# Performance work log

Hardware: AMD Instinct MI355X
Metric: run time of the kernel (lower is better)

The kernel has to match this reference:

```python
import jax, jax.numpy as jnp
import numpy as np

N_SEQ, SEQ_LEN, HIDDEN, BATCH = 2048, 128, 128, 64


def setup_inputs() -> dict:
    key = jax.random.key(0)
    ks = jax.random.split(key, 6)
    s_ih = 1.0 / np.sqrt(SEQ_LEN)
    s_hh = 1.0 / np.sqrt(HIDDEN)
    s_fc = 1.0 / np.sqrt(N_SEQ * HIDDEN)
    return {
        "x": jax.random.normal(ks[0], (BATCH, N_SEQ, SEQ_LEN), dtype=jnp.float32),
        "h0": jnp.zeros((BATCH, HIDDEN), dtype=jnp.float32),
        "c0": jnp.zeros((BATCH, HIDDEN), dtype=jnp.float32),
        # LSTM weights, PyTorch gate order (i, f, g, o) packed on last axis
        "W_ih": jax.random.uniform(ks[1], (SEQ_LEN, 4 * HIDDEN), jnp.float32, -s_ih, s_ih),
        "W_hh": jax.random.uniform(ks[2], (HIDDEN, 4 * HIDDEN), jnp.float32, -s_hh, s_hh),
        "b": jax.random.uniform(ks[3], (4 * HIDDEN,), jnp.float32, -s_ih, s_ih),
        "fc_w": jax.random.uniform(ks[4], (2, N_SEQ * HIDDEN), jnp.float32, -s_fc, s_fc),
        "fc_b": jax.random.uniform(ks[5], (2,), jnp.float32, -s_fc, s_fc),
    }


def _lstm(x_tmajor, h0, c0, W_ih, W_hh, b):
    # x_tmajor: [T, B, D]. Precompute input projection in one big matmul.
    pre = jnp.einsum("tbd,dg->tbg", x_tmajor, W_ih) + b  # [T, B, 4H]
    H = h0.shape[-1]

    def step(carry, pre_t):
        h, c = carry
        gates = pre_t + h @ W_hh  # [B, 4H]
        i = jax.nn.sigmoid(gates[:, 0 * H:1 * H])
        f = jax.nn.sigmoid(gates[:, 1 * H:2 * H])
        g = jnp.tanh(gates[:, 2 * H:3 * H])
        o = jax.nn.sigmoid(gates[:, 3 * H:4 * H])
        c_new = f * c + i * g
        h_new = o * jnp.tanh(c_new)
        return (h_new, c_new), h_new

    (_, _), hs = jax.lax.scan(step, (h0, c0), pre)
    return hs  # [T, B, H]


def reference(x, h0, c0, W_ih, W_hh, b, fc_w, fc_b):
    xt = jnp.transpose(x, (1, 0, 2))              # [T, B, D]
    hs = _lstm(xt, h0, c0, W_ih, W_hh, b)          # [T, B, H]
    hb = jnp.transpose(hs, (1, 0, 2))              # [B, T, H]
    flat = hb.reshape(hb.shape[0], -1)             # [B, T*H]
    return flat @ fc_w.T + fc_b                    # [B, 2]
```

## Files before the change

kernel.cpp:

```cpp
#include <hip/hip_runtime.h>

#define T_SEQ 2048
#define NBATCH 64
#define DIM 128
#define HID 128
#define G4 512
#define GRP 16
#define TT 16
#define LOG2E 1.44269504088896f

typedef _Float16 h2v   __attribute__((ext_vector_type(2)));
typedef _Float16 f16x8 __attribute__((ext_vector_type(8)));
typedef float    f32x4 __attribute__((ext_vector_type(4)));

__device__ __forceinline__ unsigned pack2(float lo, float hi) {
    h2v v; v.x = (_Float16)lo; v.y = (_Float16)hi;
    return __builtin_bit_cast(unsigned, v);
}
__device__ __forceinline__ float dot2(unsigned a, unsigned b, float c) {
#if __has_builtin(__builtin_amdgcn_fdot2)
    return __builtin_amdgcn_fdot2(__builtin_bit_cast(h2v, a),
                                  __builtin_bit_cast(h2v, b), c, false);
#else
    h2v av = __builtin_bit_cast(h2v, a), bv = __builtin_bit_cast(h2v, b);
    c = fmaf((float)av.x, (float)bv.x, c);
    return fmaf((float)av.y, (float)bv.y, c);
#endif
}
__device__ __forceinline__ float rcp_(float x)  { return __builtin_amdgcn_rcpf(x); }
__device__ __forceinline__ float exp2_(float x) { return __builtin_amdgcn_exp2f(x); }
template <int CTRL>
__device__ __forceinline__ float qmov(float v) {
    int r = __builtin_amdgcn_mov_dpp(__builtin_bit_cast(int, v), CTRL, 0xF, 0xF, true);
    return __builtin_bit_cast(float, r);
}
#define QP_XOR1 0xB1
#define QP_XOR2 0x4E
#define QP_B0   0x00
#define QP_B1   0x55
#define QP_B2   0xAA
#define QP_B3   0xFF

__device__ __forceinline__ void barrier_lgkm() {
    asm volatile("s_waitcnt lgkmcnt(0)\n\ts_barrier" ::: "memory");
    __builtin_amdgcn_sched_barrier(0);
}

__global__ __launch_bounds__(256) void prep(
    const float* __restrict__ x,
    const float* __restrict__ Wih,
    const float* __restrict__ Whh,
    const float* __restrict__ bias,
    _Float16* __restrict__ x16,
    _Float16* __restrict__ aXf,
    unsigned* __restrict__ whh_pk,
    float* __restrict__ bias_s)
{
    const size_t gtid   = (size_t)blockIdx.x * blockDim.x + threadIdx.x;
    const size_t stride = (size_t)gridDim.x * blockDim.x;

    const size_t n_x2 = (size_t)NBATCH * T_SEQ * DIM / 2;
    for (size_t i = gtid; i < n_x2; i += stride) {
        float2 v = reinterpret_cast<const float2*>(x)[i];
        h2v p; p.x = (_Float16)v.x; p.y = (_Float16)v.y;
        reinterpret_cast<h2v*>(x16)[i] = p;
    }
    for (size_t n = gtid; n < 65536; n += stride) {
        int i  = (int)n & 7;
        int l  = ((int)n >> 3) & 63;
        int ks = ((int)n >> 9) & 3;
        int j  = ((int)n >> 11) & 3;
        int w  = (int)n >> 13;
        int col = l & 15, hi = l >> 4;
        int chr  = 16 * (4 * w + j) + col;
        int wcol = (chr & 3) * HID + (chr >> 2);
        float sc = ((chr & 3) == 2) ? -2.0f * LOG2E : -LOG2E;
        int k = ks * 32 + hi * 8 + i;
        aXf[n] = (_Float16)(Wih[(size_t)k * G4 + wcol] * sc);
    }
    for (size_t n = gtid; n < 32768; n += stride) {
        int tid = (int)n & 511;
        int gi  = (int)n >> 9;
        int g = gi >> 4, ii = gi & 15;
        int j = tid >> 2, q = tid & 3;
        int k0 = q * 32 + 2 * ii;
        float sc = (g == 2) ? -2.0f * LOG2E : -LOG2E;
        whh_pk[n] = pack2(Whh[(size_t)k0 * G4 + g * HID + j] * sc,
                          Whh[(size_t)(k0 + 1) * G4 + g * HID + j] * sc);
    }
    for (size_t n = gtid; n < 512; n += stride) {
        int gate = (int)n & 3, u = (int)n >> 2;
        float sc = (gate == 2) ? -2.0f * LOG2E : -LOG2E;
        bias_s[n] = bias[gate * HID + u] * sc;
    }
}

__global__ __launch_bounds__(512, 2) void pre_mfma(
    const _Float16* __restrict__ x16,
    const _Float16* __restrict__ aXf,
    const float* __restrict__ bias_s,
    _Float16* __restrict__ pre,
    int t0)
{
    const int tid = threadIdx.x;
    const int w   = tid >> 6;
    const int l   = tid & 63;
    const int col = l & 15;
    const int hi  = l >> 4;
    const int bg  = blockIdx.x & 3;
    const int lt0 = (blockIdx.x >> 2) * TT;
    const int batch = bg * 16 + col;

    f16x8 aX[4][4];
    f32x4 bv[4];
    #pragma unroll
    for (int j = 0; j < 4; ++j) {
        #pragma unroll
        for (int ks = 0; ks < 4; ++ks)
            aX[j][ks] = *reinterpret_cast<const f16x8*>(
                aXf + (((size_t)(w * 4 + j) * 4 + ks) << 9) + l * 8);
        bv[j] = *reinterpret_cast<const f32x4*>(bias_s + 64 * w + 16 * j + 4 * hi);
    }

    const _Float16* xb_base = x16 + (size_t)batch * T_SEQ * DIM + hi * 8;

    for (int tt = 0; tt < TT; ++tt) {
        const int lt = lt0 + tt;
        const int t  = t0 + lt;
        f16x8 xf[4];
        #pragma unroll
        for (int ks = 0; ks < 4; ++ks)
            xf[ks] = *reinterpret_cast<const f16x8*>(
                xb_base + (size_t)t * DIM + ks * 32);
        #pragma unroll
        for (int j = 0; j < 4; ++j) {
            f32x4 acc = bv[j];
            #pragma unroll
            for (int ks = 0; ks < 4; ++ks)
                acc = __builtin_amdgcn_mfma_f32_16x16x32_f16(aX[j][ks], xf[ks], acc, 0, 0, 0);
            uint2 o;
            o.x = pack2(acc[0], acc[1]);
            o.y = pack2(acc[2], acc[3]);
            *reinterpret_cast<uint2*>(
                pre + ((size_t)lt * NBATCH + batch) * G4 + 16 * (4 * w + j) + 4 * hi) = o;
        }
    }
}

__global__ __launch_bounds__(512, 1) void lstm_scan(
    const _Float16* __restrict__ pre,
    const unsigned* __restrict__ whh_pk,
    const float* __restrict__ h0,
    const float* __restrict__ c0,
    float* __restrict__ state,
    _Float16* __restrict__ trace,
    int t0, int tc)
{
    __shared__ __align__(16) _Float16 h_sh[2][HID];

    const int tid = threadIdx.x;
    const int j = tid >> 2;
    const int q = tid & 3;
    const int b = blockIdx.x;
    const bool q1 = (q & 1) != 0;
    const bool q2 = (q & 2) != 0;

    float* st_h = state;
    float* st_c = state + NBATCH * HID;

    unsigned wpk[4][16];
    #pragma unroll
    for (int g = 0; g < 4; ++g)
        #pragma unroll
        for (int ii = 0; ii < 16; ++ii)
            wpk[g][ii] = whh_pk[(size_t)(g * 16 + ii) * 512 + tid];

    float c, hj;
    if (t0 == 0) {
        hj = h0[b * HID + j]; c = c0[b * HID + j];
    } else {
        hj = st_h[b * HID + j];
        c  = st_c[b * HID + j];
    }
    if (q == 0) h_sh[0][j] = (_Float16)hj;

    const size_t pstep = (size_t)NBATCH * G4;
    const _Float16* pb = pre + (size_t)b * G4 + tid;
    _Float16* tb = trace + ((size_t)b * T_SEQ + t0) * HID + j;

    unsigned short prA[GRP], prB[GRP];
    #pragma unroll
    for (int s = 0; s < GRP; ++s)
        prA[s] = __builtin_bit_cast(unsigned short, pb[(size_t)s * pstep]);

    __syncthreads();

#define LOADG(PR, TGN)                                                       \
    {                                                                        \
        const int tgl = (TGN);                                               \
        _Pragma("unroll")                                                    \
        for (int s = 0; s < GRP; ++s)                                        \
            PR[s] = __builtin_bit_cast(unsigned short,                       \
                        pb[(size_t)(tgl + s) * pstep]);                      \
    }

#define STEP16(PR, TG)                                                       \
    _Pragma("unroll")                                                        \
    for (int s = 0; s < GRP; ++s) {                                          \
        const int cur = s & 1;                                               \
        const uint4* hp = reinterpret_cast<const uint4*>(&h_sh[cur][q * 32]);\
        float a0 = 0.f, a1 = 0.f, a2 = 0.f, a3 = 0.f;                        \
        _Pragma("unroll")                                                    \
        for (int m = 0; m < 4; ++m) {                                        \
            uint4 hv = hp[m];                                                \
            a0 = dot2(hv.x, wpk[0][4 * m + 0], a0);                          \
            a1 = dot2(hv.x, wpk[1][4 * m + 0], a1);                          \
            a2 = dot2(hv.x, wpk[2][4 * m + 0], a2);                          \
            a3 = dot2(hv.x, wpk[3][4 * m + 0], a3);                          \
            a0 = dot2(hv.y, wpk[0][4 * m + 1], a0);                          \
            a1 = dot2(hv.y, wpk[1][4 * m + 1], a1);                          \
            a2 = dot2(hv.y, wpk[2][4 * m + 1], a2);                          \
            a3 = dot2(hv.y, wpk[3][4 * m + 1], a3);                          \
            a0 = dot2(hv.z, wpk[0][4 * m + 2], a0);                          \
            a1 = dot2(hv.z, wpk[1][4 * m + 2], a1);                          \
            a2 = dot2(hv.z, wpk[2][4 * m + 2], a2);                          \
            a3 = dot2(hv.z, wpk[3][4 * m + 2], a3);                          \
            a0 = dot2(hv.w, wpk[0][4 * m + 3], a0);                          \
            a1 = dot2(hv.w, wpk[1][4 * m + 3], a1);                          \
            a2 = dot2(hv.w, wpk[2][4 * m + 3], a2);                          \
            a3 = dot2(hv.w, wpk[3][4 * m + 3], a3);                          \
        }                                                                    \
        float t01  = q1 ? a1 : a0;                                           \
        float t01o = q1 ? a0 : a1;                                           \
        t01 += qmov<QP_XOR1>(t01o);                                          \
        float t23  = q1 ? a3 : a2;                                           \
        float t23o = q1 ? a2 : a3;                                           \
        t23 += qmov<QP_XOR1>(t23o);                                          \
        float tq  = q2 ? t23 : t01;                                          \
        float tqo = q2 ? t01 : t23;                                          \
        tq += qmov<QP_XOR2>(tqo);                                            \
        tq += (float)__builtin_bit_cast(_Float16, PR[s]);                    \
        float v = rcp_(1.0f + exp2_(tq));                                    \
        float gi = qmov<QP_B0>(v);                                           \
        float gf = qmov<QP_B1>(v);                                           \
        float vg = qmov<QP_B2>(v);                                           \
        float go = qmov<QP_B3>(v);                                           \
        c = fmaf(gf, c, fmaf(gi + gi, vg, -gi));                             \
        float vc = rcp_(1.0f + exp2_(-2.0f * LOG2E * c));                    \
        float hn = fmaf(go + go, vc, -go);                                   \
        hj = hn;                                                             \
        _Float16 h16 = (_Float16)hn;                                         \
        if (q == 0) {                                                        \
            h_sh[cur ^ 1][j] = h16;                                          \
            tb[(size_t)((TG) + s) * HID] = h16;                              \
        }                                                                    \
        barrier_lgkm();                                                      \
    }

    for (int tg = 0; tg < tc; tg += 2 * GRP) {
        LOADG(prB, tg + GRP);
        STEP16(prA, tg);
        const int tga = (tg + 2 * GRP < tc) ? tg + 2 * GRP : tg;
        LOADG(prA, tga);
        STEP16(prB, tg + GRP);
    }
#undef LOADG
#undef STEP16

    if (t0 + tc < T_SEQ) {
        if (q == 0) { st_h[b * HID + j] = hj; st_c[b * HID + j] = c; }
    }
}

__global__ __launch_bounds__(256) void fc_part(
    const _Float16* __restrict__ trace,
    const float* __restrict__ fcw,
    float* __restrict__ part)
{
    __shared__ float red[4][2];
    const int b = blockIdx.x, ck = blockIdx.y, tid = threadIdx.x;
    const int n4 = T_SEQ * HID / 4;
    const int base = ck * n4;
    const _Float16* tbase = trace + (size_t)b * (T_SEQ * HID) + base;
    const float* w0 = fcw + base;
    const float* w1 = fcw + (size_t)T_SEQ * HID + base;

    float s0 = 0.f, s1 = 0.f;
    for (int i = tid * 8; i < n4; i += 256 * 8) {
        uint4 tv = *reinterpret_cast<const uint4*>(tbase + i);
        float wa0[8], wa1[8];
        *reinterpret_cast<float4*>(&wa0[0]) = *reinterpret_cast<const float4*>(w0 + i);
        *reinterpret_cast<float4*>(&wa0[4]) = *reinterpret_cast<const float4*>(w0 + i + 4);
        *reinterpret_cast<float4*>(&wa1[0]) = *reinterpret_cast<const float4*>(w1 + i);
        *reinterpret_cast<float4*>(&wa1[4]) = *reinterpret_cast<const float4*>(w1 + i + 4);
        const unsigned* tw = reinterpret_cast<const unsigned*>(&tv);
        #pragma unroll
        for (int e = 0; e < 4; ++e) {
            h2v hh = __builtin_bit_cast(h2v, tw[e]);
            float hx = (float)hh.x, hy = (float)hh.y;
            s0 = fmaf(hx, wa0[2 * e], s0);
            s0 = fmaf(hy, wa0[2 * e + 1], s0);
            s1 = fmaf(hx, wa1[2 * e], s1);
            s1 = fmaf(hy, wa1[2 * e + 1], s1);
        }
    }
    #pragma unroll
    for (int d = 32; d >= 1; d >>= 1) {
        s0 += __shfl_xor(s0, d);
        s1 += __shfl_xor(s1, d);
    }
    const int w = tid >> 6;
    if ((tid & 63) == 0) { red[w][0] = s0; red[w][1] = s1; }
    __syncthreads();
    if (tid < 2) {
        part[(b * 4 + ck) * 2 + tid] =
            red[0][tid] + red[1][tid] + red[2][tid] + red[3][tid];
    }
}

__global__ __launch_bounds__(128) void fc_fin(
    const float* __restrict__ part,
    const float* __restrict__ fcb,
    float* __restrict__ out)
{
    const int tid = threadIdx.x;
    const int b = tid >> 1, o = tid & 1;
    float v = part[(b * 4 + 0) * 2 + o] + part[(b * 4 + 1) * 2 + o]
            + part[(b * 4 + 2) * 2 + o] + part[(b * 4 + 3) * 2 + o];
    out[b * 2 + o] = v + fcb[o];
}

extern "C" void kernel_launch(void* const* d_in, const int* in_sizes, int n_in,
                              void* d_out, int out_size, void* d_ws, size_t ws_size,
                              hipStream_t stream) {
    const float* x    = (const float*)d_in[0];
    const float* h0   = (const float*)d_in[1];
    const float* c0   = (const float*)d_in[2];
    const float* Wih  = (const float*)d_in[3];
    const float* Whh  = (const float*)d_in[4];
    const float* bias = (const float*)d_in[5];
    const float* fcw  = (const float*)d_in[6];
    const float* fcb  = (const float*)d_in[7];
    float* out = (float*)d_out;

    char* wsb = (char*)d_ws;
    const size_t X = (size_t)NBATCH * T_SEQ * DIM * 2;
    _Float16* x16    = (_Float16*)wsb;
    _Float16* trace  = (_Float16*)(wsb + X);
    float*    state  = (float*)(wsb + 2 * X);
    float*    part   = (float*)(wsb + 2 * X + 65536);
    _Float16* aXf    = (_Float16*)(wsb + 2 * X + 65536 + 2048);
    unsigned* whh_pk = (unsigned*)(wsb + 2 * X + 65536 + 2048 + 131072);
    float*    bias_s = (float*)(wsb + 2 * X + 65536 + 2048 + 2 * 131072);
    _Float16* pre    = (_Float16*)(wsb + 2 * X + 65536 + 2048 + 2 * 131072 + 2048);

    const size_t head = 2 * X + 65536 + 2048 + 2 * 131072 + 2048;
    const size_t per_t_bytes = (size_t)NBATCH * G4 * sizeof(_Float16);
    size_t avail = (ws_size > head) ? ws_size - head : 0;
    int Tc = (int)(avail / per_t_bytes);
    Tc &= ~(2 * GRP - 1);
    if (Tc < 2 * GRP) Tc = 2 * GRP;
    if (Tc > T_SEQ) Tc = T_SEQ;

    prep<<<512, 256, 0, stream>>>(x, Wih, Whh, bias, x16, aXf, whh_pk, bias_s);
    for (int t0 = 0; t0 < T_SEQ; t0 += Tc) {
        int tc = (t0 + Tc <= T_SEQ) ? Tc : (T_SEQ - t0);
        pre_mfma<<<(tc / TT) * 4, 512, 0, stream>>>(x16, aXf, bias_s, pre, t0);
        lstm_scan<<<64, 512, 0, stream>>>(pre, whh_pk, h0, c0, state, trace, t0, tc);
    }
    fc_part<<<dim3(64, 4), 256, 0, stream>>>(trace, fcw, part);
    fc_fin<<<1, 128, 0, stream>>>(part, fcb, out);
}
```

Measured before the change: 1.076 ms.

## Split LSTM recurrent matvec across 8 lanes per hidden unit with 1024-thread blocks

The recurrent scan now uses 1024 threads per batch block, with 8 lanes per hidden unit (4 gates times 2 K-halves) instead of 4, so each lane holds 32 packed weights and does 32 dot2 ops per step instead of 64. The cross-lane reduction changes from gate-transposing quad swaps to a single xor-1 add, and gates are broadcast through a half-row mirror DPP. Weight packing in prep is reordered to match. This shortens the serial per-step latency chain. In exchange it doubles the waves taking part in every per-step barrier and adds more redundant lanes.

```diff
diff --git a/kernel.cpp b/kernel.cpp
--- a/kernel.cpp
+++ b/kernel.cpp
@@ -35,11 +35,9 @@
     return __builtin_bit_cast(float, r);
 }
 #define QP_XOR1 0xB1
-#define QP_XOR2 0x4E
 #define QP_B0   0x00
-#define QP_B1   0x55
 #define QP_B2   0xAA
-#define QP_B3   0xFF
+#define DPP_HMIR 0x141
 
 __device__ __forceinline__ void barrier_lgkm() {
     asm volatile("s_waitcnt lgkmcnt(0)\n\ts_barrier" ::: "memory");
@@ -53,7 +51,7 @@
     const float* __restrict__ bias,
     _Float16* __restrict__ x16,
     _Float16* __restrict__ aXf,
-    unsigned* __restrict__ whh_pk,
+    unsigned* __restrict__ whh_pk8,
     float* __restrict__ bias_s)
 {
     const size_t gtid   = (size_t)blockIdx.x * blockDim.x + threadIdx.x;
@@ -79,14 +77,14 @@
         aXf[n] = (_Float16)(Wih[(size_t)k * G4 + wcol] * sc);
     }
     for (size_t n = gtid; n < 32768; n += stride) {
-        int tid = (int)n & 511;
-        int gi  = (int)n >> 9;
-        int g = gi >> 4, ii = gi & 15;
-        int j = tid >> 2, q = tid & 3;
-        int k0 = q * 32 + 2 * ii;
+        int tid = (int)n & 1023;
+        int wi  = (int)n >> 10;
+        int j = tid >> 3, s = tid & 7;
+        int g = s >> 1, kh = s & 1;
+        int k0 = kh * 64 + 2 * wi;
         float sc = (g == 2) ? -2.0f * LOG2E : -LOG2E;
-        whh_pk[n] = pack2(Whh[(size_t)k0 * G4 + g * HID + j] * sc,
-                          Whh[(size_t)(k0 + 1) * G4 + g * HID + j] * sc);
+        whh_pk8[n] = pack2(Whh[(size_t)k0 * G4 + g * HID + j] * sc,
+                           Whh[(size_t)(k0 + 1) * G4 + g * HID + j] * sc);
     }
     for (size_t n = gtid; n < 512; n += stride) {
         int gate = (int)n & 3, u = (int)n >> 2;
@@ -147,9 +145,9 @@
     }
 }
 
-__global__ __launch_bounds__(512, 1) void lstm_scan(
+__global__ __launch_bounds__(1024, 1) void lstm_scan(
     const _Float16* __restrict__ pre,
-    const unsigned* __restrict__ whh_pk,
+    const unsigned* __restrict__ whh_pk8,
     const float* __restrict__ h0,
     const float* __restrict__ c0,
     float* __restrict__ state,
@@ -159,21 +157,18 @@
     __shared__ __align__(16) _Float16 h_sh[2][HID];
 
     const int tid = threadIdx.x;
-    const int j = tid >> 2;
-    const int q = tid & 3;
+    const int j  = tid >> 3;
+    const int s  = tid & 7;
+    const int kh = s & 1;
     const int b = blockIdx.x;
-    const bool q1 = (q & 1) != 0;
-    const bool q2 = (q & 2) != 0;
 
     float* st_h = state;
     float* st_c = state + NBATCH * HID;
 
-    unsigned wpk[4][16];
+    unsigned wpk[32];
     #pragma unroll
-    for (int g = 0; g < 4; ++g)
-        #pragma unroll
-        for (int ii = 0; ii < 16; ++ii)
-            wpk[g][ii] = whh_pk[(size_t)(g * 16 + ii) * 512 + tid];
+    for (int i = 0; i < 32; ++i)
+        wpk[i] = whh_pk8[(size_t)i * 1024 + tid];
 
     float c, hj;
     if (t0 == 0) {
@@ -182,16 +177,16 @@
         hj = st_h[b * HID + j];
         c  = st_c[b * HID + j];
     }
-    if (q == 0) h_sh[0][j] = (_Float16)hj;
+    if (s == 0) h_sh[0][j] = (_Float16)hj;
 
     const size_t pstep = (size_t)NBATCH * G4;
-    const _Float16* pb = pre + (size_t)b * G4 + tid;
+    const _Float16* pb = pre + (size_t)b * G4 + 4 * j + (s >> 1);
     _Float16* tb = trace + ((size_t)b * T_SEQ + t0) * HID + j;
 
     unsigned short prA[GRP], prB[GRP];
     #pragma unroll
-    for (int s = 0; s < GRP; ++s)
-        prA[s] = __builtin_bit_cast(unsigned short, pb[(size_t)s * pstep]);
+    for (int ss = 0; ss < GRP; ++ss)
+        prA[ss] = __builtin_bit_cast(unsigned short, pb[(size_t)ss * pstep]);
 
     __syncthreads();
 
@@ -199,60 +194,42 @@
     {                                                                        \
         const int tgl = (TGN);                                               \
         _Pragma("unroll")                                                    \
-        for (int s = 0; s < GRP; ++s)                                        \
-            PR[s] = __builtin_bit_cast(unsigned short,                       \
-                        pb[(size_t)(tgl + s) * pstep]);                      \
+        for (int ss = 0; ss < GRP; ++ss)                                     \
+            PR[ss] = __builtin_bit_cast(unsigned short,                      \
+                        pb[(size_t)(tgl + ss) * pstep]);                     \
     }
 
 #define STEP16(PR, TG)                                                       \
     _Pragma("unroll")                                                        \
-    for (int s = 0; s < GRP; ++s) {                                          \
-        const int cur = s & 1;                                               \
-        const uint4* hp = reinterpret_cast<const uint4*>(&h_sh[cur][q * 32]);\
+    for (int ss = 0; ss < GRP; ++ss) {                                       \
+        const int cur = ss & 1;                                              \
+        const uint4* hp = reinterpret_cast<const uint4*>(&h_sh[cur][kh * 64]);\
         float a0 = 0.f, a1 = 0.f, a2 = 0.f, a3 = 0.f;                        \
         _Pragma("unroll")                                                    \
-        for (int m = 0; m < 4; ++m) {                                        \
-            uint4 hv = hp[m];                                                \
-            a0 = dot2(hv.x, wpk[0][4 * m + 0], a0);                          \
-            a1 = dot2(hv.x, wpk[1][4 * m + 0], a1);                          \
-            a2 = dot2(hv.x, wpk[2][4 * m + 0], a2);                          \
-            a3 = dot2(hv.x, wpk[3][4 * m + 0], a3);                          \
-            a0 = dot2(hv.y, wpk[0][4 * m + 1], a0);                          \
-            a1 = dot2(hv.y, wpk[1][4 * m + 1], a1);                          \
-            a2 = dot2(hv.y, wpk[2][4 * m + 1], a2);                          \
-            a3 = dot2(hv.y, wpk[3][4 * m + 1], a3);                          \
-            a0 = dot2(hv.z, wpk[0][4 * m + 2], a0);                          \
-            a1 = dot2(hv.z, wpk[1][4 * m + 2], a1);                          \
-            a2 = dot2(hv.z, wpk[2][4 * m + 2], a2);                          \
-            a3 = dot2(hv.z, wpk[3][4 * m + 2], a3);                          \
-            a0 = dot2(hv.w, wpk[0][4 * m + 3], a0);                          \
-            a1 = dot2(hv.w, wpk[1][4 * m + 3], a1);                          \
-            a2 = dot2(hv.w, wpk[2][4 * m + 3], a2);                          \
-            a3 = dot2(hv.w, wpk[3][4 * m + 3], a3);                          \
+        for (int r = 0; r < 8; ++r) {                                        \
+            uint4 hv = hp[r];                                                \
+            a0 = dot2(hv.x, wpk[4 * r + 0], a0);                             \
+            a1 = dot2(hv.y, wpk[4 * r + 1], a1);                             \
+            a2 = dot2(hv.z, wpk[4 * r + 2], a2);                             \
+            a3 = dot2(hv.w, wpk[4 * r + 3], a3);                             \
         }                                                                    \
-        float t01  = q1 ? a1 : a0;                                           \
-        float t01o = q1 ? a0 : a1;                                           \
-        t01 += qmov<QP_XOR1>(t01o);                                          \
-        float t23  = q1 ? a3 : a2;                                           \
-        float t23o = q1 ? a2 : a3;                                           \
-        t23 += qmov<QP_XOR1>(t23o);                                          \
-        float tq  = q2 ? t23 : t01;                                          \
-        float tqo = q2 ? t01 : t23;                                          \
-        tq += qmov<QP_XOR2>(tqo);                                            \
-        tq += (float)__builtin_bit_cast(_Float16, PR[s]);                    \
+        float a = (a0 + a1) + (a2 + a3);                                     \
+        a += qmov<QP_XOR1>(a);            \
+        float tq = a + (float)__builtin_bit_cast(_Float16, PR[ss]);          \
         float v = rcp_(1.0f + exp2_(tq));                                    \
-        float gi = qmov<QP_B0>(v);                                           \
-        float gf = qmov<QP_B1>(v);                                           \
-        float vg = qmov<QP_B2>(v);                                           \
-        float go = qmov<QP_B3>(v);                                           \
+        float m = qmov<DPP_HMIR>(v);       \
+        float gi = qmov<QP_B0>(v);                                \
+        float gf = qmov<QP_B2>(v);                                \
+        float vg = qmov<QP_B2>(m);                                \
+        float go = qmov<QP_B0>(m);                                \
         c = fmaf(gf, c, fmaf(gi + gi, vg, -gi));                             \
         float vc = rcp_(1.0f + exp2_(-2.0f * LOG2E * c));                    \
         float hn = fmaf(go + go, vc, -go);                                   \
         hj = hn;                                                             \
         _Float16 h16 = (_Float16)hn;                                         \
-        if (q == 0) {                                                        \
+        if (s == 0) {                                                        \
             h_sh[cur ^ 1][j] = h16;                                          \
-            tb[(size_t)((TG) + s) * HID] = h16;                              \
+            tb[(size_t)((TG) + ss) * HID] = h16;                             \
         }                                                                    \
         barrier_lgkm();                                                      \
     }
@@ -268,7 +245,7 @@
 #undef STEP16
 
     if (t0 + tc < T_SEQ) {
-        if (q == 0) { st_h[b * HID + j] = hj; st_c[b * HID + j] = c; }
+        if (s == 0) { st_h[b * HID + j] = hj; st_c[b * HID + j] = c; }
     }
 }
 
@@ -345,14 +322,14 @@
 
     char* wsb = (char*)d_ws;
     const size_t X = (size_t)NBATCH * T_SEQ * DIM * 2;
-    _Float16* x16    = (_Float16*)wsb;
-    _Float16* trace  = (_Float16*)(wsb + X);
-    float*    state  = (float*)(wsb + 2 * X);
-    float*    part   = (float*)(wsb + 2 * X + 65536);
-    _Float16* aXf    = (_Float16*)(wsb + 2 * X + 65536 + 2048);
-    unsigned* whh_pk = (unsigned*)(wsb + 2 * X + 65536 + 2048 + 131072);
-    float*    bias_s = (float*)(wsb + 2 * X + 65536 + 2048 + 2 * 131072);
-    _Float16* pre    = (_Float16*)(wsb + 2 * X + 65536 + 2048 + 2 * 131072 + 2048);
+    _Float16* x16     = (_Float16*)wsb;
+    _Float16* trace   = (_Float16*)(wsb + X);
+    float*    state   = (float*)(wsb + 2 * X);
+    float*    part    = (float*)(wsb + 2 * X + 65536);
+    _Float16* aXf     = (_Float16*)(wsb + 2 * X + 65536 + 2048);
+    unsigned* whh_pk8 = (unsigned*)(wsb + 2 * X + 65536 + 2048 + 131072);
+    float*    bias_s  = (float*)(wsb + 2 * X + 65536 + 2048 + 2 * 131072);
+    _Float16* pre     = (_Float16*)(wsb + 2 * X + 65536 + 2048 + 2 * 131072 + 2048);
 
     const size_t head = 2 * X + 65536 + 2048 + 2 * 131072 + 2048;
     const size_t per_t_bytes = (size_t)NBATCH * G4 * sizeof(_Float16);
@@ -362,11 +339,11 @@
     if (Tc < 2 * GRP) Tc = 2 * GRP;
     if (Tc > T_SEQ) Tc = T_SEQ;
 
-    prep<<<512, 256, 0, stream>>>(x, Wih, Whh, bias, x16, aXf, whh_pk, bias_s);
+    prep<<<512, 256, 0, stream>>>(x, Wih, Whh, bias, x16, aXf, whh_pk8, bias_s);
     for (int t0 = 0; t0 < T_SEQ; t0 += Tc) {
         int tc = (t0 + Tc <= T_SEQ) ? Tc : (T_SEQ - t0);
         pre_mfma<<<(tc / TT) * 4, 512, 0, stream>>>(x16, aXf, bias_s, pre, t0);
-        lstm_scan<<<64, 512, 0, stream>>>(pre, whh_pk, h0, c0, state, trace, t0, tc);
+        lstm_scan<<<64, 1024, 0, stream>>>(pre, whh_pk8, h0, c0, state, trace, t0, tc);
     }
     fc_part<<<dim3(64, 4), 256, 0, stream>>>(trace, fcw, part);
     fc_fin<<<1, 128, 0, stream>>>(part, fcb, out);
```

New measurement: 1.333 ms. 1.24x slower.

## Process two batch rows per LSTM scan block to share weights and barriers

Applied to the files above, without the earlier changes.

Each lstm_scan block now advances two independent batch sequences in lockstep, so the grid drops from 64 to 32 blocks. The register-resident W_hh slices are reused for both GEMVs, and one barrier per timestep is shared by both sequences, which gives more independent work to hide the latency of the serial recurrence. The cost is roughly double the arithmetic per step on each CU, half as many CUs in use, and higher register pressure from the extra prefetch buffers and accumulators.

```diff
diff --git a/kernel.cpp b/kernel.cpp
--- a/kernel.cpp
+++ b/kernel.cpp
@@ -156,12 +156,13 @@
     _Float16* __restrict__ trace,
     int t0, int tc)
 {
-    __shared__ __align__(16) _Float16 h_sh[2][HID];
+    __shared__ __align__(16) _Float16 h_sh[2][2][HID];
 
     const int tid = threadIdx.x;
     const int j = tid >> 2;
     const int q = tid & 3;
-    const int b = blockIdx.x;
+    const int b0 = blockIdx.x * 2;
+    const int b1 = b0 + 1;
     const bool q1 = (q & 1) != 0;
     const bool q2 = (q & 2) != 0;
 
@@ -175,100 +176,136 @@
         for (int ii = 0; ii < 16; ++ii)
             wpk[g][ii] = whh_pk[(size_t)(g * 16 + ii) * 512 + tid];
 
-    float c, hj;
+    float cA, cB, hjA, hjB;
     if (t0 == 0) {
-        hj = h0[b * HID + j]; c = c0[b * HID + j];
+        hjA = h0[b0 * HID + j]; cA = c0[b0 * HID + j];
+        hjB = h0[b1 * HID + j]; cB = c0[b1 * HID + j];
     } else {
-        hj = st_h[b * HID + j];
-        c  = st_c[b * HID + j];
-    }
-    if (q == 0) h_sh[0][j] = (_Float16)hj;
+        hjA = st_h[b0 * HID + j]; cA = st_c[b0 * HID + j];
+        hjB = st_h[b1 * HID + j]; cB = st_c[b1 * HID + j];
+    }
+    if (q == 0) {
+        h_sh[0][0][j] = (_Float16)hjA;
+        h_sh[0][1][j] = (_Float16)hjB;
+    }
 
     const size_t pstep = (size_t)NBATCH * G4;
-    const _Float16* pb = pre + (size_t)b * G4 + tid;
-    _Float16* tb = trace + ((size_t)b * T_SEQ + t0) * HID + j;
-
-    unsigned short prA[GRP], prB[GRP];
+    const _Float16* pbA = pre + (size_t)b0 * G4 + tid;
+    const _Float16* pbB = pre + (size_t)b1 * G4 + tid;
+    _Float16* tbA = trace + ((size_t)b0 * T_SEQ + t0) * HID + j;
+    _Float16* tbB = trace + ((size_t)b1 * T_SEQ + t0) * HID + j;
+
+    unsigned short pA0[GRP], pA1[GRP], pB0[GRP], pB1[GRP];
     #pragma unroll
-    for (int s = 0; s < GRP; ++s)
-        prA[s] = __builtin_bit_cast(unsigned short, pb[(size_t)s * pstep]);
+    for (int s = 0; s < GRP; ++s) {
+        pA0[s] = __builtin_bit_cast(unsigned short, pbA[(size_t)s * pstep]);
+        pA1[s] = __builtin_bit_cast(unsigned short, pbB[(size_t)s * pstep]);
+    }
 
     __syncthreads();
 
-#define LOADG(PR, TGN)                                                       \
+#define LOADG(P0, P1, TGN)                                                   \
     {                                                                        \
         const int tgl = (TGN);                                               \
         _Pragma("unroll")                                                    \
-        for (int s = 0; s < GRP; ++s)                                        \
-            PR[s] = __builtin_bit_cast(unsigned short,                       \
-                        pb[(size_t)(tgl + s) * pstep]);                      \
-    }
-
-#define STEP16(PR, TG)                                                       \
-    _Pragma("unroll")                                                        \
-    for (int s = 0; s < GRP; ++s) {                                          \
-        const int cur = s & 1;                                               \
-        const uint4* hp = reinterpret_cast<const uint4*>(&h_sh[cur][q * 32]);\
-        float a0 = 0.f, a1 = 0.f, a2 = 0.f, a3 = 0.f;                        \
+        for (int s = 0; s < GRP; ++s) {                                      \
+            P0[s] = __builtin_bit_cast(unsigned short,                       \
+                        pbA[(size_t)(tgl + s) * pstep]);                     \
+            P1[s] = __builtin_bit_cast(unsigned short,                       \
+                        pbB[(size_t)(tgl + s) * pstep]);                     \
+        }                                                                    \
+    }
+
+#define GEMV(HP, A0, A1, A2, A3)                                             \
+    {                                                                        \
         _Pragma("unroll")                                                    \
         for (int m = 0; m < 4; ++m) {                                        \
-            uint4 hv = hp[m];                                                \
-            a0 = dot2(hv.x, wpk[0][4 * m + 0], a0);                          \
-            a1 = dot2(hv.x, wpk[1][4 * m + 0], a1);                          \
-            a2 = dot2(hv.x, wpk[2][4 * m + 0], a2);                          \
-            a3 = dot2(hv.x, wpk[3][4 * m + 0], a3);                          \
-            a0 = dot2(hv.y, wpk[0][4 * m + 1], a0);                          \
-            a1 = dot2(hv.y, wpk[1][4 * m + 1], a1);                          \
-            a2 = dot2(hv.y, wpk[2][4 * m + 1], a2);                          \
-            a3 = dot2(hv.y, wpk[3][4 * m + 1], a3);                          \
-            a0 = dot2(hv.z, wpk[0][4 * m + 2], a0);                          \
-            a1 = dot2(hv.z, wpk[1][4 * m + 2], a1);                          \
-            a2 = dot2(hv.z, wpk[2][4 * m + 2], a2);                          \
-            a3 = dot2(hv.z, wpk[3][4 * m + 2], a3);                          \
-            a0 = dot2(hv.w, wpk[0][4 * m + 3], a0);                          \
-            a1 = dot2(hv.w, wpk[1][4 * m + 3], a1);                          \
-            a2 = dot2(hv.w, wpk[2][4 * m + 3], a2);                          \
-            a3 = dot2(hv.w, wpk[3][4 * m + 3], a3);                          \
+            uint4 hv = (HP)[m];                                              \
+            A0 = dot2(hv.x, wpk[0][4 * m + 0], A0);                          \
+            A1 = dot2(hv.x, wpk[1][4 * m + 0], A1);                          \
+            A2 = dot2(hv.x, wpk[2][4 * m + 0], A2);                          \
+            A3 = dot2(hv.x, wpk[3][4 * m + 0], A3);                          \
+            A0 = dot2(hv.y, wpk[0][4 * m + 1], A0);                          \
+            A1 = dot2(hv.y, wpk[1][4 * m + 1], A1);                          \
+            A2 = dot2(hv.y, wpk[2][4 * m + 1], A2);                          \
+            A3 = dot2(hv.y, wpk[3][4 * m + 1], A3);                          \
+            A0 = dot2(hv.z, wpk[0][4 * m + 2], A0);                          \
+            A1 = dot2(hv.z, wpk[1][4 * m + 2], A1);                          \
+            A2 = dot2(hv.z, wpk[2][4 * m + 2], A2);                          \
+            A3 = dot2(hv.z, wpk[3][4 * m + 2], A3);                          \
+            A0 = dot2(hv.w, wpk[0][4 * m + 3], A0);                          \
+            A1 = dot2(hv.w, wpk[1][4 * m + 3], A1);                          \
+            A2 = dot2(hv.w, wpk[2][4 * m + 3], A2);                          \
+            A3 = dot2(hv.w, wpk[3][4 * m + 3], A3);                          \
         }                                                                    \
-        float t01  = q1 ? a1 : a0;                                           \
-        float t01o = q1 ? a0 : a1;                                           \
+    }
+
+#define EPI(A0, A1, A2, A3, PRV, CV, HJ)                                     \
+    float hn_;                                                               \
+    {                                                                        \
+        float t01  = q1 ? A1 : A0;                                           \
+        float t01o = q1 ? A0 : A1;                                           \
         t01 += qmov<QP_XOR1>(t01o);                                          \
-        float t23  = q1 ? a3 : a2;                                           \
-        float t23o = q1 ? a2 : a3;                                           \
+        float t23  = q1 ? A3 : A2;                                           \
+        float t23o = q1 ? A2 : A3;                                           \
         t23 += qmov<QP_XOR1>(t23o);                                          \
         float tq  = q2 ? t23 : t01;                                          \
         float tqo = q2 ? t01 : t23;                                          \
         tq += qmov<QP_XOR2>(tqo);                                            \
-        tq += (float)__builtin_bit_cast(_Float16, PR[s]);                    \
+        tq += (float)__builtin_bit_cast(_Float16, PRV);                      \
         float v = rcp_(1.0f + exp2_(tq));                                    \
         float gi = qmov<QP_B0>(v);                                           \
         float gf = qmov<QP_B1>(v);                                           \
         float vg = qmov<QP_B2>(v);                                           \
         float go = qmov<QP_B3>(v);                                           \
-        c = fmaf(gf, c, fmaf(gi + gi, vg, -gi));                             \
-        float vc = rcp_(1.0f + exp2_(-2.0f * LOG2E * c));                    \
-        float hn = fmaf(go + go, vc, -go);                                   \
-        hj = hn;                                                             \
-        _Float16 h16 = (_Float16)hn;                                         \
-        if (q == 0) {                                                        \
-            h_sh[cur ^ 1][j] = h16;                                          \
-            tb[(size_t)((TG) + s) * HID] = h16;                              \
-        }                                                                    \
+        CV = fmaf(gf, CV, fmaf(gi + gi, vg, -gi));                           \
+        float vc = rcp_(1.0f + exp2_(-2.0f * LOG2E * CV));                   \
+        hn_ = fmaf(go + go, vc, -go);                                        \
+        HJ = hn_;                                                            \
+    }
+
+#define STEP16(P0, P1, TG)                                                   \
+    _Pragma("unroll")                                                        \
+    for (int ss = 0; ss < GRP; ++ss) {                                       \
+        const int cur = ss & 1;                                              \
+        const uint4* hpA = reinterpret_cast<const uint4*>(&h_sh[cur][0][q * 32]); \
+        const uint4* hpB = reinterpret_cast<const uint4*>(&h_sh[cur][1][q * 32]); \
+        float a0 = 0.f, a1 = 0.f, a2 = 0.f, a3 = 0.f;                        \
+        float e0 = 0.f, e1 = 0.f, e2 = 0.f, e3 = 0.f;                        \
+        GEMV(hpA, a0, a1, a2, a3);                                           \
+        GEMV(hpB, e0, e1, e2, e3);                                           \
+        { EPI(a0, a1, a2, a3, P0[ss], cA, hjA)                               \
+          if (q == 0) {                                                      \
+              _Float16 h16 = (_Float16)hn_;                                  \
+              h_sh[cur ^ 1][0][j] = h16;                                     \
+              tbA[(size_t)((TG) + ss) * HID] = h16;                          \
+          } }                                                                \
+        { EPI(e0, e1, e2, e3, P1[ss], cB, hjB)                               \
+          if (q == 0) {                                                      \
+              _Float16 h16 = (_Float16)hn_;                                  \
+              h_sh[cur ^ 1][1][j] = h16;                                     \
+              tbB[(size_t)((TG) + ss) * HID] = h16;                          \
+          } }                                                                \
         barrier_lgkm();                                                      \
     }
 
     for (int tg = 0; tg < tc; tg += 2 * GRP) {
-        LOADG(prB, tg + GRP);
-        STEP16(prA, tg);
+        LOADG(pB0, pB1, tg + GRP);
+        STEP16(pA0, pA1, tg);
         const int tga = (tg + 2 * GRP < tc) ? tg + 2 * GRP : tg;
-        LOADG(prA, tga);
-        STEP16(prB, tg + GRP);
+        LOADG(pA0, pA1, tga);
+        STEP16(pB0, pB1, tg + GRP);
     }
 #undef LOADG
+#undef GEMV
+#undef EPI
 #undef STEP16
 
     if (t0 + tc < T_SEQ) {
-        if (q == 0) { st_h[b * HID + j] = hj; st_c[b * HID + j] = c; }
+        if (q == 0) {
+            st_h[b0 * HID + j] = hjA; st_c[b0 * HID + j] = cA;
+            st_h[b1 * HID + j] = hjB; st_c[b1 * HID + j] = cB;
+        }
     }
 }
 
@@ -366,7 +403,7 @@
     for (int t0 = 0; t0 < T_SEQ; t0 += Tc) {
         int tc = (t0 + Tc <= T_SEQ) ? Tc : (T_SEQ - t0);
         pre_mfma<<<(tc / TT) * 4, 512, 0, stream>>>(x16, aXf, bias_s, pre, t0);
-        lstm_scan<<<64, 512, 0, stream>>>(pre, whh_pk, h0, c0, state, trace, t0, tc);
+        lstm_scan<<<32, 512, 0, stream>>>(pre, whh_pk, h0, c0, state, trace, t0, tc);
     }
     fc_part<<<dim3(64, 4), 256, 0, stream>>>(trace, fcw, part);
     fc_fin<<<1, 128, 0, stream>>>(part, fcb, out);
```

New measurement: 1.930 ms. 79.4% more time.
